# Kernel tuning notes

Measured on AMD Instinct MI355X. Metric: run time of the kernel, lower is better.

## Reference

```python
import jax, jax.numpy as jnp
import numpy as np
from jax import lax

CAP_SIZE = 8
N_IN, N_OUT, OUT_SIZE = 144, 10, 16
ROUTING_ITERS = 3
DN = ('NCHW', 'OIHW', 'NCHW')


def setup_inputs() -> dict:
    key = jax.random.key(0)
    ks = jax.random.split(key, 6)
    B = 2048
    inp = {
        'input': jax.random.uniform(ks[0], (B, 1, 28, 28), dtype=jnp.float32),
        'conv1_w': jax.random.normal(ks[1], (16, 1, 9, 9), dtype=jnp.float32) * 0.1,
        'conv1_b': jnp.zeros((16,), dtype=jnp.float32),
        'conv2_w': jax.random.normal(ks[2], (32, 16, 9, 9), dtype=jnp.float32) * 0.05,
        'conv2_b': jnp.zeros((32,), dtype=jnp.float32),
        'W_route': jax.random.normal(ks[3], (N_IN, N_OUT, OUT_SIZE, CAP_SIZE), dtype=jnp.float32) * 0.1,
    }
    return inp


def squash(s, axis=-1, eps=1e-8):
    sq = jnp.sum(jnp.square(s), axis=axis, keepdims=True)
    return (sq / (1.0 + sq)) * s / jnp.sqrt(sq + eps)


def reference(input, conv1_w, conv1_b, conv2_w, conv2_b, W_route):
    # PrimaryCaps: two valid convs
    x = lax.conv_general_dilated(input, conv1_w, (1, 1), 'VALID', dimension_numbers=DN)
    x = x + conv1_b[None, :, None, None]                      # [B,16,20,20]
    x = lax.conv_general_dilated(x, conv2_w, (2, 2), 'VALID', dimension_numbers=DN)
    x = x + conv2_b[None, :, None, None]                      # [B,32,6,6]
    B = x.shape[0]
    u = jnp.transpose(x.reshape(B, CAP_SIZE, -1), (0, 2, 1))  # [B,144,8]

    # prediction vectors u_hat[b,i,j,:] = W[i,j] @ u[b,i]
    u_hat = jnp.einsum('iojc,bic->bioj', W_route, u)          # [B,144,10,16]

    # routing-by-agreement
    b_log = jnp.zeros((B, N_IN, N_OUT), dtype=u_hat.dtype)
    for _ in range(ROUTING_ITERS):
        c = jax.nn.softmax(b_log, axis=2)                     # couple over out caps
        s = jnp.einsum('bio,biod->bod', c, u_hat)             # [B,10,16]
        v = squash(s)                                         # [B,10,16]
        b_log = b_log + jnp.einsum('biod,bod->bio', u_hat, v)

    pred = jnp.sqrt(jnp.sum(jnp.square(v), axis=-1))          # [B,10]
    return (pred, v)
```

## Files before the change

kernel.cpp:

```cpp
#include <hip/hip_runtime.h>


typedef _Float16 half2_t __attribute__((ext_vector_type(2)));
typedef _Float16 f16x4 __attribute__((ext_vector_type(4)));
typedef _Float16 f16x8 __attribute__((ext_vector_type(8)));
typedef float f32x16 __attribute__((ext_vector_type(16)));

static __device__ __forceinline__ float fdot2f(half2_t a, half2_t b, float c) {
#if __has_builtin(__builtin_amdgcn_fdot2)
  return __builtin_amdgcn_fdot2(a, b, c, false);
#else
  return c + (float)a[0] * (float)b[0] + (float)a[1] * (float)b[1];
#endif
}

static __device__ __forceinline__ half2_t h2(unsigned int u) {
  return __builtin_bit_cast(half2_t, u);
}

static __device__ __forceinline__ unsigned int pkh2(float a, float b) {
  half2_t h;
  h[0] = (_Float16)a;
  h[1] = (_Float16)b;
  return __builtin_bit_cast(unsigned int, h);
}

static __device__ __forceinline__ f32x16 zero16() {
  f32x16 z = {0.f, 0.f, 0.f, 0.f, 0.f, 0.f, 0.f, 0.f,
              0.f, 0.f, 0.f, 0.f, 0.f, 0.f, 0.f, 0.f};
  return z;
}

__global__ __launch_bounds__(256) void packAll(
    const float* __restrict__ w2, const float* __restrict__ Wr,
    _Float16* __restrict__ wBg, unsigned int* __restrict__ wPr) {
  int idx = blockIdx.x * 256 + threadIdx.x;
  if (idx < 92160) {
    int cp = idx & 3;
    int row = idx >> 2;
    const float* src = Wr + (size_t)row * 8 + cp * 2;
    wPr[idx] = pkh2(src[0], src[1]);
  }
  if (idx < 41472) {
    int j = idx & 7;
    int lane = (idx >> 3) & 63;
    int step = idx >> 9;
    int kh = step / 9, kw = step - kh * 9;
    int co = lane & 31, ci = (lane >> 5) * 8 + j;
    wBg[idx] = (_Float16)w2[(co * 16 + ci) * 81 + kh * 9 + kw];
  }
}

__global__ __launch_bounds__(320) void conv_fused(
    const float* __restrict__ in, const float* __restrict__ w,
    const float* __restrict__ bias1, const _Float16* __restrict__ wBg,
    const float* __restrict__ bias2, float* __restrict__ u) {
  __shared__ __align__(16) float sIn[784];
  __shared__ float sW[1296];
  __shared__ __align__(16) _Float16 sOut[8000];
  int b = blockIdx.x, t = threadIdx.x;
  const float* inb = in + b * 784;
  for (int i = t; i < 784; i += 320) sIn[i] = inb[i];
  for (int i = t; i < 1296; i += 320) sW[i] = w[i];
  __syncthreads();
  {
    int oh = t >> 4, co = t & 15;
    float bv = bias1[co];
    float acc[20];
#pragma unroll
    for (int j = 0; j < 20; ++j) acc[j] = bv;
#pragma unroll
    for (int kh = 0; kh < 9; ++kh) {
      float r[28];
      const float4* row = (const float4*)&sIn[(oh + kh) * 28];
#pragma unroll
      for (int q = 0; q < 7; ++q) {
        float4 v = row[q];
        r[q * 4 + 0] = v.x; r[q * 4 + 1] = v.y; r[q * 4 + 2] = v.z; r[q * 4 + 3] = v.w;
      }
      const float* wr = &sW[co * 81 + kh * 9];
#pragma unroll
      for (int kw = 0; kw < 9; ++kw) {
        float wv = wr[kw];
#pragma unroll
        for (int j = 0; j < 20; ++j) acc[j] += wv * r[kw + j];
      }
    }
#pragma unroll
    for (int j = 0; j < 20; ++j) sOut[(oh * 20 + j) * 20 + co] = (_Float16)acc[j];
  }
  __syncthreads();

  int wv = t >> 6, lane = t & 63;
  if (wv < 2) {
    int l31 = lane & 31, half = lane >> 5;
    int r = wv * 32 + l31;
    int rc = (r < 36) ? r : 35;
    int oh = rc / 6, ow = rc - oh * 6;
    int tb = (oh * 40 + ow * 2) * 20 + half * 8;
    f32x16 acc = zero16();
    for (int kh = 0; kh < 9; ++kh) {
      int abase = tb + kh * 400;
#pragma unroll
      for (int kw = 0; kw < 9; ++kw) {
        f16x8 bf = *(const f16x8*)(wBg + ((kh * 9 + kw) * 64 + lane) * 8);
        const _Float16* ap = sOut + abase + kw * 20;
        f16x4 lo = *(const f16x4*)ap;
        f16x4 hi = *(const f16x4*)(ap + 4);
        f16x8 a = __builtin_shufflevector(lo, hi, 0, 1, 2, 3, 4, 5, 6, 7);
        acc = __builtin_amdgcn_mfma_f32_32x32x16_f16(a, bf, acc, 0, 0, 0);
      }
    }
    float bv = bias2[l31];
    int c8 = l31 >> 2;
    int ibco = (l31 & 3) * 36;
    float* ub = u + (size_t)b * 1152;
#pragma unroll
    for (int reg = 0; reg < 16; ++reg) {
      int rr = wv * 32 + (reg & 3) + 8 * (reg >> 2) + 4 * half;
      if (rr < 36) ub[(ibco + rr) * 8 + c8] = acc[reg] + bv;
    }
  }
}

__global__ __launch_bounds__(1024) void routing2_kernel(
    const float* __restrict__ u, const unsigned int* __restrict__ wPr,
    float* __restrict__ out, int B) {
  __shared__ unsigned int uhh[2][11808];
  __shared__ unsigned int ush[2][576];
  __shared__ float cc[2][1440];
  __shared__ float spart[2][12][160];
  __shared__ float vv[2][160];
  __shared__ unsigned int vvh[2][80];
  int b0 = blockIdx.x * 2, t = threadIdx.x;
  for (int j = t; j < 1152; j += 1024) {
    int sl2 = j / 576, k = j - sl2 * 576;
    float2 p = *(const float2*)(u + (size_t)(b0 + sl2) * 1152 + k * 2);
    ush[sl2][k] = pkh2(p.x, p.y);
  }
  __syncthreads();

  bool act = t < 960;
  int chf = t / 80, dpf = t - (t / 80) * 80;
  if (act) {
    const uint4* W4 = (const uint4*)wPr;
    int rowoff = (dpf >> 3) * 16 + (dpf & 7) * 2;
    int ibase = chf * 12;
    float sA0 = 0.f, sA1 = 0.f, sB0 = 0.f, sB1 = 0.f;
    uint4 w0a = W4[ibase * 160 + rowoff];
    uint4 w1a = W4[ibase * 160 + rowoff + 1];
#pragma unroll
    for (int e = 0; e < 12; ++e) {
      int i = ibase + e;
      uint4 w0b, w1b;
      if (e < 11) {
        w0b = W4[(i + 1) * 160 + rowoff];
        w1b = W4[(i + 1) * 160 + rowoff + 1];
      }
      {
        const uint2* up = (const uint2*)&ush[0][i * 4];
        uint2 ua = up[0], ub = up[1];
        half2_t u0 = h2(ua.x), u1 = h2(ua.y), u2 = h2(ub.x), u3 = h2(ub.y);
        float a0 = fdot2f(h2(w0a.x), u0,
                   fdot2f(h2(w0a.y), u1,
                   fdot2f(h2(w0a.z), u2, fdot2f(h2(w0a.w), u3, 0.f))));
        float a1 = fdot2f(h2(w1a.x), u0,
                   fdot2f(h2(w1a.y), u1,
                   fdot2f(h2(w1a.z), u2, fdot2f(h2(w1a.w), u3, 0.f))));
        uhh[0][i * 82 + dpf] = pkh2(a0, a1);
        sA0 += a0; sA1 += a1;
      }
      {
        const uint2* up = (const uint2*)&ush[1][i * 4];
        uint2 ua = up[0], ub = up[1];
        half2_t u0 = h2(ua.x), u1 = h2(ua.y), u2 = h2(ub.x), u3 = h2(ub.y);
        float a0 = fdot2f(h2(w0a.x), u0,
                   fdot2f(h2(w0a.y), u1,
                   fdot2f(h2(w0a.z), u2, fdot2f(h2(w0a.w), u3, 0.f))));
        float a1 = fdot2f(h2(w1a.x), u0,
                   fdot2f(h2(w1a.y), u1,
                   fdot2f(h2(w1a.z), u2, fdot2f(h2(w1a.w), u3, 0.f))));
        uhh[1][i * 82 + dpf] = pkh2(a0, a1);
        sB0 += a0; sB1 += a1;
      }
      w0a = w0b; w1a = w1b;
    }
    spart[0][chf][dpf * 2] = sA0;
    spart[0][chf][dpf * 2 + 1] = sA1;
    spart[1][chf][dpf * 2] = sB0;
    spart[1][chf][dpf * 2 + 1] = sB1;
  }
  __syncthreads();

  int sl = t >> 9, tl = t & 511;
  bool bown = t < 288;
  int slb = t / 144, ib = t - (t / 144) * 144;
  float breg[10];
#pragma unroll
  for (int o = 0; o < 10; ++o) breg[o] = 0.f;

  for (int it = 0; it < 3; ++it) {
    if (it > 0) {
      if (bown) {
        float mx = breg[0];
#pragma unroll
        for (int o = 1; o < 10; ++o) mx = fmaxf(mx, breg[o]);
        float e[10];
        float sum = 0.f;
#pragma unroll
        for (int o = 0; o < 10; ++o) { e[o] = __expf(breg[o] - mx); sum += e[o]; }
        float inv = 1.0f / sum;
#pragma unroll
        for (int o = 0; o < 10; ++o) cc[slb][ib * 10 + o] = e[o] * inv;
      }
      __syncthreads();
      if (tl < 480) {
        int ch = tl / 80, dp = tl - ch * 80;
        int o = dp >> 3;
        float a0 = 0.f, a1 = 0.f;
        int i0 = ch * 24;
        for (int i = i0; i < i0 + 24; ++i) {
          float c = cc[sl][i * 10 + o];
          half2_t h = h2(uhh[sl][i * 82 + dp]);
          a0 += c * (float)h[0]; a1 += c * (float)h[1];
        }
        spart[sl][ch][dp * 2] = a0;
        spart[sl][ch][dp * 2 + 1] = a1;
      }
      __syncthreads();
    }
    if (tl < 160) {
      float s = 0.f;
      if (it == 0) {
#pragma unroll
        for (int c = 0; c < 12; ++c) s += spart[sl][c][tl];
        s *= 0.1f;
      } else {
#pragma unroll
        for (int c = 0; c < 6; ++c) s += spart[sl][c][tl];
      }
      float sq = s * s;
      sq += __shfl_xor(sq, 1);
      sq += __shfl_xor(sq, 2);
      sq += __shfl_xor(sq, 4);
      sq += __shfl_xor(sq, 8);
      float coef = (sq / (1.0f + sq)) / sqrtf(sq + 1e-8f);
      float v = coef * s;
      vv[sl][tl] = v;
      float vn = __shfl_xor(v, 1);
      if ((tl & 1) == 0) vvh[sl][tl >> 1] = pkh2(v, vn);
      if (it == 2 && (tl & 15) == 0)
        out[(b0 + sl) * 10 + (tl >> 4)] = coef * sqrtf(sq);
    }
    __syncthreads();
    if (it < 2 && bown) {
      const uint2* row = (const uint2*)&uhh[slb][ib * 82];
      const uint2* vp = (const uint2*)&vvh[slb][0];
#pragma unroll
      for (int o = 0; o < 10; ++o) {
        uint2 A0 = row[o * 4 + 0], A1 = row[o * 4 + 1];
        uint2 A2 = row[o * 4 + 2], A3 = row[o * 4 + 3];
        uint2 V0 = vp[o * 4 + 0], V1 = vp[o * 4 + 1];
        uint2 V2 = vp[o * 4 + 2], V3 = vp[o * 4 + 3];
        float da = fdot2f(h2(A0.x), h2(V0.x), fdot2f(h2(A0.y), h2(V0.y), 0.f));
        float db = fdot2f(h2(A1.x), h2(V1.x), fdot2f(h2(A1.y), h2(V1.y), 0.f));
        da = fdot2f(h2(A2.x), h2(V2.x), fdot2f(h2(A2.y), h2(V2.y), da));
        db = fdot2f(h2(A3.x), h2(V3.x), fdot2f(h2(A3.y), h2(V3.y), db));
        breg[o] += da + db;
      }
    }
  }
  if (tl < 160) out[B * 10 + (b0 + sl) * 160 + tl] = vv[sl][tl];
}

extern "C" void kernel_launch(void* const* d_in, const int* in_sizes, int n_in,
                              void* d_out, int out_size, void* d_ws, size_t ws_size,
                              hipStream_t stream) {
  const float* in = (const float*)d_in[0];
  const float* w1 = (const float*)d_in[1];
  const float* b1 = (const float*)d_in[2];
  const float* w2 = (const float*)d_in[3];
  const float* b2 = (const float*)d_in[4];
  const float* Wr = (const float*)d_in[5];
  float* out = (float*)d_out;
  int B = in_sizes[0] / 784;
  float* wsf = (float*)d_ws;

  float* u = wsf;
  float* tail = wsf + (size_t)B * 1152;
  _Float16* wBg = (_Float16*)tail;
  unsigned int* wPr = (unsigned int*)(tail + 20736);

  packAll<<<360, 256, 0, stream>>>(w2, Wr, wBg, wPr);
  conv_fused<<<B, 320, 0, stream>>>(in, w1, b1, wBg, b2, u);
  routing2_kernel<<<B / 2, 1024, 0, stream>>>(u, wPr, out, B);
}
```

Baseline: 92.31 us.

## Fuse conv stages and capsule routing into a single two-sample kernel

```diff
diff --git a/kernel.cpp b/kernel.cpp
--- a/kernel.cpp
+++ b/kernel.cpp
@@ -51,20 +51,35 @@
   }
 }
 
-__global__ __launch_bounds__(320) void conv_fused(
-    const float* __restrict__ in, const float* __restrict__ w,
+__global__ __launch_bounds__(1024) void capsnet_fused(
+    const float* __restrict__ in, const float* __restrict__ w1g,
     const float* __restrict__ bias1, const _Float16* __restrict__ wBg,
-    const float* __restrict__ bias2, float* __restrict__ u) {
-  __shared__ __align__(16) float sIn[784];
-  __shared__ float sW[1296];
-  __shared__ __align__(16) _Float16 sOut[8000];
-  int b = blockIdx.x, t = threadIdx.x;
-  const float* inb = in + b * 784;
-  for (int i = t; i < 784; i += 320) sIn[i] = inb[i];
-  for (int i = t; i < 1296; i += 320) sW[i] = w[i];
-  __syncthreads();
-  {
-    int oh = t >> 4, co = t & 15;
+    const float* __restrict__ bias2, const unsigned int* __restrict__ wPr,
+    float* __restrict__ out, int B) {
+  __shared__ __align__(16) unsigned char smemA[94464];
+  __shared__ unsigned int ush[2][576];
+  __shared__ float cc[2][1440];
+  __shared__ float spart[2][12][160];
+  __shared__ float vv[2][160];
+  __shared__ unsigned int vvh[2][80];
+  float* sIn = (float*)smemA;
+  float* sW = (float*)(smemA + 6272);
+  _Float16* sOut = (_Float16*)(smemA + 11456);
+  unsigned int* uhh0 = (unsigned int*)smemA;
+  unsigned int* uhh1 = (unsigned int*)(smemA + 47232);
+
+  int b0 = blockIdx.x * 2, t = threadIdx.x;
+  for (int j = t; j < 1568; j += 1024) {
+    int s = j / 784, k = j - s * 784;
+    sIn[j] = in[(size_t)(b0 + s) * 784 + k];
+  }
+  for (int j = t; j < 1296; j += 1024) sW[j] = w1g[j];
+  __syncthreads();
+
+  if (t < 640) {
+    int s = (t >= 320) ? 1 : 0;
+    int tt = t - s * 320;
+    int oh = tt >> 4, co = tt & 15;
     float bv = bias1[co];
     float acc[20];
 #pragma unroll
@@ -72,11 +87,12 @@
 #pragma unroll
     for (int kh = 0; kh < 9; ++kh) {
       float r[28];
-      const float4* row = (const float4*)&sIn[(oh + kh) * 28];
+      const float4* row = (const float4*)&sIn[s * 784 + (oh + kh) * 28];
 #pragma unroll
       for (int q = 0; q < 7; ++q) {
         float4 v = row[q];
-        r[q * 4 + 0] = v.x; r[q * 4 + 1] = v.y; r[q * 4 + 2] = v.z; r[q * 4 + 3] = v.w;
+        r[q * 4 + 0] = v.x; r[q * 4 + 1] = v.y;
+        r[q * 4 + 2] = v.z; r[q * 4 + 3] = v.w;
       }
       const float* wr = &sW[co * 81 + kh * 9];
 #pragma unroll
@@ -87,17 +103,19 @@
       }
     }
 #pragma unroll
-    for (int j = 0; j < 20; ++j) sOut[(oh * 20 + j) * 20 + co] = (_Float16)acc[j];
-  }
-  __syncthreads();
-
-  int wv = t >> 6, lane = t & 63;
-  if (wv < 2) {
+    for (int j = 0; j < 20; ++j)
+      sOut[s * 8000 + (oh * 20 + j) * 20 + co] = (_Float16)acc[j];
+  }
+  __syncthreads();
+
+  int wvv = t >> 6, lane = t & 63;
+  if (wvv < 4) {
+    int s = wvv >> 1, tile = wvv & 1;
     int l31 = lane & 31, half = lane >> 5;
-    int r = wv * 32 + l31;
+    int r = tile * 32 + l31;
     int rc = (r < 36) ? r : 35;
     int oh = rc / 6, ow = rc - oh * 6;
-    int tb = (oh * 40 + ow * 2) * 20 + half * 8;
+    int tb = s * 8000 + (oh * 40 + ow * 2) * 20 + half * 8;
     f32x16 acc = zero16();
     for (int kh = 0; kh < 9; ++kh) {
       int abase = tb + kh * 400;
@@ -114,29 +132,12 @@
     float bv = bias2[l31];
     int c8 = l31 >> 2;
     int ibco = (l31 & 3) * 36;
-    float* ub = u + (size_t)b * 1152;
+    _Float16* ushf = (_Float16*)&ush[s][0];
 #pragma unroll
     for (int reg = 0; reg < 16; ++reg) {
-      int rr = wv * 32 + (reg & 3) + 8 * (reg >> 2) + 4 * half;
-      if (rr < 36) ub[(ibco + rr) * 8 + c8] = acc[reg] + bv;
-    }
-  }
-}
-
-__global__ __launch_bounds__(1024) void routing2_kernel(
-    const float* __restrict__ u, const unsigned int* __restrict__ wPr,
-    float* __restrict__ out, int B) {
-  __shared__ unsigned int uhh[2][11808];
-  __shared__ unsigned int ush[2][576];
-  __shared__ float cc[2][1440];
-  __shared__ float spart[2][12][160];
-  __shared__ float vv[2][160];
-  __shared__ unsigned int vvh[2][80];
-  int b0 = blockIdx.x * 2, t = threadIdx.x;
-  for (int j = t; j < 1152; j += 1024) {
-    int sl2 = j / 576, k = j - sl2 * 576;
-    float2 p = *(const float2*)(u + (size_t)(b0 + sl2) * 1152 + k * 2);
-    ush[sl2][k] = pkh2(p.x, p.y);
+      int rr = tile * 32 + (reg & 3) + 8 * (reg >> 2) + 4 * half;
+      if (rr < 36) ushf[(ibco + rr) * 8 + c8] = (_Float16)(acc[reg] + bv);
+    }
   }
   __syncthreads();
 
@@ -167,7 +168,7 @@
         float a1 = fdot2f(h2(w1a.x), u0,
                    fdot2f(h2(w1a.y), u1,
                    fdot2f(h2(w1a.z), u2, fdot2f(h2(w1a.w), u3, 0.f))));
-        uhh[0][i * 82 + dpf] = pkh2(a0, a1);
+        uhh0[i * 82 + dpf] = pkh2(a0, a1);
         sA0 += a0; sA1 += a1;
       }
       {
@@ -180,7 +181,7 @@
         float a1 = fdot2f(h2(w1a.x), u0,
                    fdot2f(h2(w1a.y), u1,
                    fdot2f(h2(w1a.z), u2, fdot2f(h2(w1a.w), u3, 0.f))));
-        uhh[1][i * 82 + dpf] = pkh2(a0, a1);
+        uhh1[i * 82 + dpf] = pkh2(a0, a1);
         sB0 += a0; sB1 += a1;
       }
       w0a = w0b; w1a = w1b;
@@ -193,8 +194,10 @@
   __syncthreads();
 
   int sl = t >> 9, tl = t & 511;
+  unsigned int* uhsl = (sl == 0) ? uhh0 : uhh1;
   bool bown = t < 288;
   int slb = t / 144, ib = t - (t / 144) * 144;
+  unsigned int* uhb = (slb == 0) ? uhh0 : uhh1;
   float breg[10];
 #pragma unroll
   for (int o = 0; o < 10; ++o) breg[o] = 0.f;
@@ -221,7 +224,7 @@
         int i0 = ch * 24;
         for (int i = i0; i < i0 + 24; ++i) {
           float c = cc[sl][i * 10 + o];
-          half2_t h = h2(uhh[sl][i * 82 + dp]);
+          half2_t h = h2(uhsl[i * 82 + dp]);
           a0 += c * (float)h[0]; a1 += c * (float)h[1];
         }
         spart[sl][ch][dp * 2] = a0;
@@ -254,7 +257,7 @@
     }
     __syncthreads();
     if (it < 2 && bown) {
-      const uint2* row = (const uint2*)&uhh[slb][ib * 82];
+      const uint2* row = (const uint2*)&uhb[ib * 82];
       const uint2* vp = (const uint2*)&vvh[slb][0];
 #pragma unroll
       for (int o = 0; o < 10; ++o) {
@@ -286,12 +289,9 @@
   int B = in_sizes[0] / 784;
   float* wsf = (float*)d_ws;
 
-  float* u = wsf;
-  float* tail = wsf + (size_t)B * 1152;
-  _Float16* wBg = (_Float16*)tail;
-  unsigned int* wPr = (unsigned int*)(tail + 20736);
+  _Float16* wBg = (_Float16*)wsf;
+  unsigned int* wPr = (unsigned int*)(wsf + 20736);
 
   packAll<<<360, 256, 0, stream>>>(w2, Wr, wBg, wPr);
-  conv_fused<<<B, 320, 0, stream>>>(in, w1, b1, wBg, b2, u);
-  routing2_kernel<<<B / 2, 1024, 0, stream>>>(u, wPr, out, B);
-}
+  capsnet_fused<<<B / 2, 1024, 0, stream>>>(in, w1, b1, wBg, b2, wPr, out, B);
+}
```

After: 92.22 us. About the same (-0.1%).
